# Performance work log

Measured on AMD Instinct MI355X. Metric: run time of the kernel, lower is better.

## Reference

```python
import jax, jax.numpy as jnp
import numpy as np
from jax import lax

# SLAYER neuron / simulation constants (from netParams)
THETA = 10.0       # spike threshold
TAU_SR = 10.0      # synaptic (PSP) time constant
TAU_REF = 1.0      # refractory time constant
SCALE_REF = 2.0    # refractory scale
TAU_RHO = 1.0      # surrogate-gradient width (unused in fwd)
K_PSP = 32         # truncation length of SRM alpha kernel
K_REF = 16         # truncation length of refractory kernel

_t = np.arange(K_PSP, dtype=np.float64)
PSP_KERN = jnp.asarray((_t / TAU_SR) * np.exp(1.0 - _t / TAU_SR), jnp.float32)  # [K_PSP]
_tr = np.arange(1, K_REF + 1, dtype=np.float64)
REF_KERN = jnp.asarray(-SCALE_REF * THETA * (_tr / TAU_REF) * np.exp(1.0 - _tr / TAU_REF), jnp.float32)  # [K_REF]


def psp(x):
    """Causal temporal FIR filter with SRM alpha kernel; x: [..., T]."""
    sh = x.shape
    T = sh[-1]
    flat = x.reshape(-1, 1, T)                       # [B*, 1, T]
    k = PSP_KERN[::-1][None, None, :]                # correlation kernel (reversed)
    y = lax.conv_general_dilated(flat, k, (1,), [(K_PSP - 1, 0)])
    return y.reshape(sh)


def spike(u):
    """Threshold with refractory feedback, sequential over time. u: [..., T]."""
    uT = jnp.moveaxis(u, -1, 0)                      # [T, ...]
    buf0 = jnp.zeros(u.shape[:-1] + (K_REF,), u.dtype)

    def step(buf, ut):
        v = ut + buf[..., 0]
        s = (v >= THETA).astype(u.dtype)
        buf = jnp.concatenate([buf[..., 1:], jnp.zeros_like(buf[..., :1])], -1)
        buf = buf + s[..., None] * REF_KERN
        return buf, s

    _, sT = lax.scan(step, buf0, uT)
    return jnp.moveaxis(sT, 0, -1)


def conv_t(x, w, stride, pad):
    """2D conv applied independently per timestep. x: [N,C,H,W,T], w: [Co,C,kh,kw]."""
    N, C, H, W, T = x.shape
    xt = jnp.moveaxis(x, -1, 1).reshape(N * T, C, H, W)
    y = lax.conv_general_dilated(xt, w, (stride, stride), [(pad, pad), (pad, pad)])
    Co, Ho, Wo = y.shape[1], y.shape[2], y.shape[3]
    return jnp.moveaxis(y.reshape(N, T, Co, Ho, Wo), 1, -1)


def pool_t(x):
    """SLAYER sum-pool 2x2/s2 with weight 1.1*theta/kernel_area. x: [N,C,H,W,T]."""
    s = lax.reduce_window(x, np.float32(0.0), lax.add, (1, 1, 2, 2, 1), (1, 1, 2, 2, 1), 'VALID')
    return s * np.float32(1.1 * THETA / 4.0)


def setup_inputs() -> dict:
    key = jax.random.key(0)
    ks = jax.random.split(key, 5)
    spikeInput = (jax.random.uniform(ks[0], (4, 2, 256, 256, 50)) < 0.02).astype(jnp.float32)
    w1 = jax.random.normal(ks[1], (8, 2, 5, 5), jnp.float32) * 2.0
    w2 = jax.random.normal(ks[2], (16, 8, 3, 3), jnp.float32) * 1.5
    w3 = jax.random.normal(ks[3], (32, 16, 3, 3), jnp.float32) * 1.5
    w_fc = jax.random.normal(ks[4], (2, 32, 8, 8), jnp.float32) * 0.3
    return {"spikeInput": spikeInput, "w1": w1, "w2": w2, "w3": w3, "w_fc": w_fc}


def reference(spikeInput, w1, w2, w3, w_fc):
    x = spike(conv_t(psp(spikeInput), w1, 2, 1))   # [4,8,127,127,50]
    x = spike(pool_t(psp(x)))                      # [4,8,63,63,50]
    x = spike(conv_t(psp(x), w2, 2, 1))            # [4,16,32,32,50]
    x = spike(pool_t(psp(x)))                      # [4,16,16,16,50]
    x = spike(conv_t(psp(x), w3, 2, 1))            # [4,32,8,8,50]
    u = psp(x)
    out = jnp.einsum('ochw,nchwt->not', w_fc, u)   # dense over (C,H,W)
    return spike(out[:, :, None, None, :])         # [4,2,1,1,50]
```

## Files before the change

### kernel.cpp

```cpp
#include <hip/hip_runtime.h>
#include <cmath>

struct K32 { float k[32]; };
struct K16 { float k[16]; };

#define THETA 10.0f

__global__ __launch_bounds__(128)
void psp_kernel(const float* __restrict__ in, float* __restrict__ out,
                int nrows, K32 pk) {
  __shared__ __align__(16) float lds[64 * 50];
  const int rowBase = blockIdx.x * 64;
  const int tid = threadIdx.x;
  const int vr = min(64, nrows - rowBase);
  const int n4 = (vr * 50) >> 2;
  const float4* g4 = (const float4*)(in + (size_t)rowBase * 50);
  for (int i = tid; i < n4; i += 128) *(float4*)(&lds[4 * i]) = g4[i];
  __syncthreads();
  const int r = tid & 63;
  const int part = tid >> 6;
  const bool act = r < vr;
  float x[50];
  if (act) {
    if (part == 0) {
#pragma unroll
      for (int t = 0; t < 25; ++t) x[t] = lds[r * 50 + t];
    } else {
#pragma unroll
      for (int t = 0; t < 50; ++t) x[t] = lds[r * 50 + t];
    }
  }
  __syncthreads();
  if (act) {
    if (part == 0) {
#pragma unroll
      for (int t = 0; t < 25; ++t) {
        float a = 0.f;
#pragma unroll
        for (int k = 31; k >= 0; --k)
          if (t - k >= 0) a += x[t - k] * pk.k[k];
        lds[r * 50 + t] = a;
      }
    } else {
#pragma unroll
      for (int t = 25; t < 50; ++t) {
        float a = 0.f;
#pragma unroll
        for (int k = 31; k >= 0; --k)
          if (t - k >= 0) a += x[t - k] * pk.k[k];
        lds[r * 50 + t] = a;
      }
    }
  }
  __syncthreads();
  float4* o4 = (float4*)(out + (size_t)rowBase * 50);
  for (int i = tid; i < n4; i += 128) o4[i] = *(const float4*)(&lds[4 * i]);
}

template <int CIN, int COUT, int KK, int WT, int HIN, int WIN, int HOUT, int WOUT>
__global__ __launch_bounds__(256)
void conv_spike_kernel(const float* __restrict__ x, const float* __restrict__ w,
                       float* __restrict__ s, K16 rk) {
  constexpr int XR = 2 * (WT - 1) + KK;
  constexpr int TW = 4 * WT;
  constexpr int GROUPS = (WOUT + TW - 1) / TW;
  __shared__ float lds[COUT * TW * 51];
  const int tid = threadIdx.x;
  const int wave = tid >> 6;
  const int lane = tid & 63;
  const int group = blockIdx.x % GROUPS;
  const int rest = blockIdx.x / GROUPS;
  const int ho = rest % HOUT;
  const int n = rest / HOUT;
  const int wo0 = group * TW + wave * WT;
  const int tt = lane < 50 ? lane : 49;

  float acc[COUT][WT] = {};
  for (int c = 0; c < CIN; ++c) {
#pragma unroll
    for (int kh = 0; kh < KK; ++kh) {
      const int hi = 2 * ho + kh - 1;
      if ((unsigned)hi >= (unsigned)HIN) continue;
      float xr[XR];
#pragma unroll
      for (int i = 0; i < XR; ++i) {
        const int wi = 2 * wo0 - 1 + i;
        xr[i] = ((unsigned)wi < (unsigned)WIN)
                    ? x[(((size_t)(n * CIN + c) * HIN + hi) * WIN + wi) * 50 + tt]
                    : 0.f;
      }
#pragma unroll
      for (int co = 0; co < COUT; ++co)
#pragma unroll
        for (int kw = 0; kw < KK; ++kw) {
          const float wv = w[((co * CIN + c) * KK + kh) * KK + kw];
#pragma unroll
          for (int wl = 0; wl < WT; ++wl)
            acc[co][wl] += xr[2 * wl + kw] * wv;
        }
    }
  }

  if (lane < 50) {
#pragma unroll
    for (int co = 0; co < COUT; ++co)
#pragma unroll
      for (int wl = 0; wl < WT; ++wl)
        lds[(co * TW + wave * WT + wl) * 51 + lane] = acc[co][wl];
  }
  __syncthreads();
  if (tid < COUT * TW) {
    const int co = tid / TW;
    const int wol = tid - co * TW;
    const int wo = group * TW + wol;
    if (wo < WOUT) {
      float* orow = s + (((size_t)(n * COUT + co) * HOUT + ho) * WOUT + wo) * 50;
      float buf[16];
#pragma unroll
      for (int j = 0; j < 16; ++j) buf[j] = 0.f;
      float prev = 0.f;
#pragma unroll
      for (int t = 0; t < 50; ++t) {
        float v = lds[tid * 51 + t] + buf[t & 15];
        buf[t & 15] = 0.f;
        float sp = 0.f;
        if (v >= THETA) {
          sp = 1.f;
#pragma unroll
          for (int j = 0; j < 16; ++j) buf[(t + 1 + j) & 15] += rk.k[j];
        }
        if (t & 1) *(float2*)(orow + t - 1) = make_float2(prev, sp);
        else prev = sp;
      }
    }
  }
}

__global__ __launch_bounds__(128)
void pps_kernel(const float* __restrict__ in, float* __restrict__ out,
                int Hin, int Win, int Hout, int Wout, int nseg,
                K32 pk, K16 rk) {
  __shared__ __align__(16) float lds[80 * 50];
  const int tid = threadIdx.x;
  const int seg = blockIdx.x % nseg;
  const int rest = blockIdx.x / nseg;
  const int ho = rest % Hout;
  const int nc = rest / Hout;
  const int wbase = seg * 32;
  const int nw = min(32, 2 * Wout - wbase);
  const int nwo = nw >> 1;
  const int span = nw * 50;
  const float* b0 = in + ((size_t)(nc * Hin + 2 * ho) * Win + wbase) * 50;
  const float* b1 = b0 + (size_t)Win * 50;
  const int n2 = span >> 1;
  for (int i = tid; i < n2; i += 128) {
    *(float2*)(&lds[2 * i]) = *(const float2*)(b0 + 2 * i);
    *(float2*)(&lds[span + 2 * i]) = *(const float2*)(b1 + 2 * i);
  }
  __syncthreads();
  const int r = tid & 63;
  const int part = tid >> 6;
  const bool act = r < 2 * nw;
  float x[50];
  if (act) {
    if (part == 0) {
#pragma unroll
      for (int t = 0; t < 25; ++t) x[t] = lds[r * 50 + t];
    } else {
#pragma unroll
      for (int t = 0; t < 50; ++t) x[t] = lds[r * 50 + t];
    }
  }
  __syncthreads();
  if (act) {
    if (part == 0) {
#pragma unroll
      for (int t = 0; t < 25; ++t) {
        float a = 0.f;
#pragma unroll
        for (int k = 31; k >= 0; --k)
          if (t - k >= 0) a += x[t - k] * pk.k[k];
        lds[r * 50 + t] = a;
      }
    } else {
#pragma unroll
      for (int t = 25; t < 50; ++t) {
        float a = 0.f;
#pragma unroll
        for (int k = 31; k >= 0; --k)
          if (t - k >= 0) a += x[t - k] * pk.k[k];
        lds[r * 50 + t] = a;
      }
    }
  }
  __syncthreads();
  if (tid < nwo) {
    float buf[16];
#pragma unroll
    for (int j = 0; j < 16; ++j) buf[j] = 0.f;
    const int r00 = (2 * tid) * 50, r01 = (2 * tid + 1) * 50;
    const int r10 = (nw + 2 * tid) * 50, r11 = (nw + 2 * tid + 1) * 50;
    const int ro = (2 * nw + tid) * 50;
#pragma unroll
    for (int t = 0; t < 50; ++t) {
      const float u0 = (((lds[r00 + t] + lds[r01 + t]) + lds[r10 + t]) + lds[r11 + t]) * 2.75f;
      float v = u0 + buf[t & 15];
      buf[t & 15] = 0.f;
      float sp = 0.f;
      if (v >= THETA) {
        sp = 1.f;
#pragma unroll
        for (int j = 0; j < 16; ++j) buf[(t + 1 + j) & 15] += rk.k[j];
      }
      lds[ro + t] = sp;
    }
  }
  __syncthreads();
  float* ob = out + ((size_t)(nc * Hout + ho) * Wout + seg * 16) * 50;
  const int base = 2 * nw * 50;
  for (int i = tid; i < nwo * 25; i += 128)
    *(float2*)(ob + 2 * i) = *(const float2*)(&lds[base + 2 * i]);
}

__global__ __launch_bounds__(512)
void fc_spike_kernel(const float* __restrict__ w, const float* __restrict__ u,
                     float* __restrict__ out, K16 rk) {
  __shared__ float lds[8 * 51];
  const int tid = threadIdx.x;
  const int wave = tid >> 6, lane = tid & 63;
  const int o = wave & 1, n = wave >> 1;
  const int tt = lane < 50 ? lane : 49;
  const float* wrow = w + (size_t)o * 2048;
  const float* ub = u + (size_t)n * 2048 * 50;
  float acc = 0.f;
#pragma unroll 32
  for (int i = 0; i < 2048; ++i) acc += wrow[i] * ub[(size_t)i * 50 + tt];
  if (lane < 50) lds[wave * 51 + lane] = acc;
  __syncthreads();
  if (tid < 8) {
    float buf[16];
#pragma unroll
    for (int j = 0; j < 16; ++j) buf[j] = 0.f;
#pragma unroll
    for (int t = 0; t < 50; ++t) {
      float v = lds[tid * 51 + t] + buf[t & 15];
      buf[t & 15] = 0.f;
      float sp = 0.f;
      if (v >= THETA) {
        sp = 1.f;
#pragma unroll
        for (int j = 0; j < 16; ++j) buf[(t + 1 + j) & 15] += rk.k[j];
      }
      out[tid * 50 + t] = sp;
    }
  }
}

extern "C" void kernel_launch(void* const* d_in, const int* in_sizes, int n_in,
                              void* d_out, int out_size, void* d_ws, size_t ws_size,
                              hipStream_t stream) {
  const float* xin = (const float*)d_in[0];
  const float* w1  = (const float*)d_in[1];
  const float* w2  = (const float*)d_in[2];
  const float* w3  = (const float*)d_in[3];
  const float* wfc = (const float*)d_in[4];
  float* out = (float*)d_out;

  float* R0 = (float*)d_ws;
  float* R1 = R0 + 26214400;

  K32 pk;
  for (int k = 0; k < 32; ++k)
    pk.k[k] = (float)(((double)k / 10.0) * exp(1.0 - (double)k / 10.0));
  K16 rk;
  for (int j = 0; j < 16; ++j) {
    const double tr = (double)(j + 1);
    rk.k[j] = (float)(-2.0 * 10.0 * tr * exp(1.0 - tr));
  }

  psp_kernel<<<8192, 128, 0, stream>>>(xin, R0, 524288, pk);
  conv_spike_kernel<2, 8, 5, 4, 256, 256, 127, 127>
      <<<4 * 127 * 8, 256, 0, stream>>>(R0, w1, R1, rk);
  pps_kernel<<<4 * 8 * 63 * 4, 128, 0, stream>>>(R1, R0, 127, 127, 63, 63, 4, pk, rk);
  psp_kernel<<<1985, 128, 0, stream>>>(R0, R1, 127008, pk);
  conv_spike_kernel<8, 16, 3, 1, 63, 63, 32, 32>
      <<<4 * 32 * 8, 256, 0, stream>>>(R1, w2, R0, rk);
  pps_kernel<<<4 * 16 * 16, 128, 0, stream>>>(R0, R1, 32, 32, 16, 16, 1, pk, rk);
  psp_kernel<<<256, 128, 0, stream>>>(R1, R0, 16384, pk);
  conv_spike_kernel<16, 32, 3, 1, 16, 16, 8, 8>
      <<<4 * 8 * 2, 256, 0, stream>>>(R0, w3, R1, rk);
  psp_kernel<<<128, 128, 0, stream>>>(R1, R0, 8192, pk);
  fc_spike_kernel<<<1, 512, 0, stream>>>(wfc, R0, out, rk);
}
```

Measured before the change: 531.8 us.

## Fuse layer-1 conv+spike with PSP, pooling and spike into one kernel

Adds a conv_pps_kernel that computes a 2x8 patch of layer-1 conv outputs per block, applies the spike and refractory scan in LDS, then the PSP filter, 2x2 sum-pool and a second spike. The layer-1 spike map ([4,8,127,127,50]) no longer goes to global memory and is not read back by a separate pps kernel. The fused kernel's LDS holds a 2x8 tile per output channel with 51-float padding per row. Its phases are separated by several block barriers, and only a subset of the threads is active in the scan and pool phases.

```diff
diff --git a/kernel.cpp b/kernel.cpp
--- a/kernel.cpp
+++ b/kernel.cpp
@@ -55,6 +55,155 @@
   __syncthreads();
   float4* o4 = (float4*)(out + (size_t)rowBase * 50);
   for (int i = tid; i < n4; i += 128) o4[i] = *(const float4*)(&lds[4 * i]);
+}
+
+template <int CIN, int COUT, int KK, int HIN, int WIN, int S1H, int S1W,
+          int S2H, int S2W>
+__global__ __launch_bounds__(256)
+void conv_pps_kernel(const float* __restrict__ x, const float* __restrict__ w,
+                     float* __restrict__ s2out, K32 pk, K16 rk) {
+  constexpr int WT = 4;
+  constexpr int SW = 8;
+  constexpr int XR = 2 * (WT - 1) + KK;
+  constexpr int GROUPS = (S1W + SW - 1) / SW;
+  constexpr int NROW = COUT * 2 * SW;
+  __shared__ float lds[NROW * 51];
+  const int tid = threadIdx.x;
+  const int wave = tid >> 6;
+  const int lane = tid & 63;
+  const int group = blockIdx.x % GROUPS;
+  const int rest = blockIdx.x / GROUPS;
+  const int hop = rest % S2H;
+  const int n = rest / S2H;
+  const int ho_off = wave & 1;
+  const int wo_half = wave >> 1;
+  const int ho = 2 * hop + ho_off;
+  const int wo0 = group * SW + wo_half * WT;
+  const int tt = lane < 50 ? lane : 49;
+
+  float acc[COUT][WT] = {};
+  for (int c = 0; c < CIN; ++c) {
+#pragma unroll
+    for (int kh = 0; kh < KK; ++kh) {
+      const int hi = 2 * ho + kh - 1;
+      if ((unsigned)hi >= (unsigned)HIN) continue;
+      float xr[XR];
+#pragma unroll
+      for (int i = 0; i < XR; ++i) {
+        const int wi = 2 * wo0 - 1 + i;
+        xr[i] = ((unsigned)wi < (unsigned)WIN)
+                    ? x[(((size_t)(n * CIN + c) * HIN + hi) * WIN + wi) * 50 + tt]
+                    : 0.f;
+      }
+#pragma unroll
+      for (int co = 0; co < COUT; ++co)
+#pragma unroll
+        for (int kw = 0; kw < KK; ++kw) {
+          const float wv = w[((co * CIN + c) * KK + kh) * KK + kw];
+#pragma unroll
+          for (int wl = 0; wl < WT; ++wl)
+            acc[co][wl] += xr[2 * wl + kw] * wv;
+        }
+    }
+  }
+  if (lane < 50) {
+#pragma unroll
+    for (int co = 0; co < COUT; ++co)
+#pragma unroll
+      for (int wl = 0; wl < WT; ++wl)
+        lds[((co * 2 + ho_off) * SW + wo_half * WT + wl) * 51 + lane] = acc[co][wl];
+  }
+  __syncthreads();
+  if (tid < NROW) {
+    const int wol = tid & (SW - 1);
+    if (group * SW + wol < S1W) {
+      float buf[16];
+#pragma unroll
+      for (int j = 0; j < 16; ++j) buf[j] = 0.f;
+#pragma unroll
+      for (int t = 0; t < 50; ++t) {
+        float v = lds[tid * 51 + t] + buf[t & 15];
+        buf[t & 15] = 0.f;
+        float sp = 0.f;
+        if (v >= THETA) {
+          sp = 1.f;
+#pragma unroll
+          for (int j = 0; j < 16; ++j) buf[(t + 1 + j) & 15] += rk.k[j];
+        }
+        lds[tid * 51 + t] = sp;
+      }
+    }
+  }
+  __syncthreads();
+  {
+    const int r = tid & (NROW - 1);
+    const int part = tid >> 7;
+    const int wol = r & (SW - 1);
+    const bool act = (group * SW + wol) < S1W;
+    float xs[50];
+    if (act) {
+      if (part == 0) {
+#pragma unroll
+        for (int t = 0; t < 25; ++t) xs[t] = lds[r * 51 + t];
+      } else {
+#pragma unroll
+        for (int t = 0; t < 50; ++t) xs[t] = lds[r * 51 + t];
+      }
+    }
+    __syncthreads();
+    if (act) {
+      if (part == 0) {
+#pragma unroll
+        for (int t = 0; t < 25; ++t) {
+          float a = 0.f;
+#pragma unroll
+          for (int k = 31; k >= 0; --k)
+            if (t - k >= 0) a += xs[t - k] * pk.k[k];
+          lds[r * 51 + t] = a;
+        }
+      } else {
+#pragma unroll
+        for (int t = 25; t < 50; ++t) {
+          float a = 0.f;
+#pragma unroll
+          for (int k = 31; k >= 0; --k)
+            if (t - k >= 0) a += xs[t - k] * pk.k[k];
+          lds[r * 51 + t] = a;
+        }
+      }
+    }
+  }
+  __syncthreads();
+  if (tid < COUT * (SW / 2)) {
+    const int co = tid / (SW / 2);
+    const int wpl = tid % (SW / 2);
+    const int wop = group * (SW / 2) + wpl;
+    if (wop < S2W) {
+      const int r00 = (co * 16 + 2 * wpl) * 51;
+      const int r01 = (co * 16 + 2 * wpl + 1) * 51;
+      const int r10 = (co * 16 + 8 + 2 * wpl) * 51;
+      const int r11 = (co * 16 + 8 + 2 * wpl + 1) * 51;
+      float* orow = s2out + (((size_t)(n * COUT + co) * S2H + hop) * S2W + wop) * 50;
+      float buf[16];
+#pragma unroll
+      for (int j = 0; j < 16; ++j) buf[j] = 0.f;
+      float prev = 0.f;
+#pragma unroll
+      for (int t = 0; t < 50; ++t) {
+        const float u0 = (((lds[r00 + t] + lds[r01 + t]) + lds[r10 + t]) + lds[r11 + t]) * 2.75f;
+        float v = u0 + buf[t & 15];
+        buf[t & 15] = 0.f;
+        float sp = 0.f;
+        if (v >= THETA) {
+          sp = 1.f;
+#pragma unroll
+          for (int j = 0; j < 16; ++j) buf[(t + 1 + j) & 15] += rk.k[j];
+        }
+        if (t & 1) *(float2*)(orow + t - 1) = make_float2(prev, sp);
+        else prev = sp;
+      }
+    }
+  }
 }
 
 template <int CIN, int COUT, int KK, int WT, int HIN, int WIN, int HOUT, int WOUT>
@@ -279,16 +428,15 @@
   }
 
   psp_kernel<<<8192, 128, 0, stream>>>(xin, R0, 524288, pk);
-  conv_spike_kernel<2, 8, 5, 4, 256, 256, 127, 127>
-      <<<4 * 127 * 8, 256, 0, stream>>>(R0, w1, R1, rk);
-  pps_kernel<<<4 * 8 * 63 * 4, 128, 0, stream>>>(R1, R0, 127, 127, 63, 63, 4, pk, rk);
-  psp_kernel<<<1985, 128, 0, stream>>>(R0, R1, 127008, pk);
+  conv_pps_kernel<2, 8, 5, 256, 256, 127, 127, 63, 63>
+      <<<4 * 63 * 16, 256, 0, stream>>>(R0, w1, R1, pk, rk);
+  psp_kernel<<<1985, 128, 0, stream>>>(R1, R0, 127008, pk);
   conv_spike_kernel<8, 16, 3, 1, 63, 63, 32, 32>
-      <<<4 * 32 * 8, 256, 0, stream>>>(R1, w2, R0, rk);
-  pps_kernel<<<4 * 16 * 16, 128, 0, stream>>>(R0, R1, 32, 32, 16, 16, 1, pk, rk);
-  psp_kernel<<<256, 128, 0, stream>>>(R1, R0, 16384, pk);
+      <<<4 * 32 * 8, 256, 0, stream>>>(R0, w2, R1, rk);
+  pps_kernel<<<4 * 16 * 16, 128, 0, stream>>>(R1, R0, 32, 32, 16, 16, 1, pk, rk);
+  psp_kernel<<<256, 128, 0, stream>>>(R0, R1, 16384, pk);
   conv_spike_kernel<16, 32, 3, 1, 16, 16, 8, 8>
-      <<<4 * 8 * 2, 256, 0, stream>>>(R0, w3, R1, rk);
-  psp_kernel<<<128, 128, 0, stream>>>(R1, R0, 8192, pk);
-  fc_spike_kernel<<<1, 512, 0, stream>>>(wfc, R0, out, rk);
-}
+      <<<4 * 8 * 2, 256, 0, stream>>>(R1, w3, R0, rk);
+  psp_kernel<<<128, 128, 0, stream>>>(R0, R1, 8192, pk);
+  fc_spike_kernel<<<1, 512, 0, stream>>>(wfc, R1, out, rk);
+}
```

New measurement: 506.4 us, median of 3. 1.05x faster.
